# Kernel tuning notes

Hardware: AMD Instinct MI355X
Metric: run time of the kernel (lower is better)

Reference implementation:

```python
import jax, jax.numpy as jnp
import numpy as np

N = 8192
IN_DIM = 64
OUT_DIM = 64
HEADS = 2
EPS = 1e-10


def setup_inputs() -> dict:
    key = jax.random.key(0)
    ks = jax.random.split(key, 6)
    features = jax.random.normal(ks[0], (N, IN_DIM), dtype=jnp.float32)
    adj = (jax.random.uniform(ks[1], (N, N)) < 0.005).astype(jnp.float32)
    # per-head attention linear: Linear(2*in_dim, 1) stacked -> [heads, 2*in_dim]
    W_attn = jax.random.normal(ks[2], (HEADS, 2 * IN_DIM), dtype=jnp.float32) * 0.05
    b_attn = jax.random.normal(ks[3], (HEADS,), dtype=jnp.float32) * 0.05
    # feature transform: Linear(in_dim, heads*out_dim)
    W_lin = jax.random.normal(ks[4], (HEADS * OUT_DIM, IN_DIM), dtype=jnp.float32) * 0.05
    b_lin = jax.random.normal(ks[5], (HEADS * OUT_DIM,), dtype=jnp.float32) * 0.05
    return {"adj": adj, "features": features, "W_attn": W_attn,
            "b_attn": b_attn, "W_lin": W_lin, "b_lin": b_lin}


def reference(adj, features, W_attn, b_attn, W_lin, b_lin):
    n, in_dim = features.shape
    heads = W_attn.shape[0]
    # add self-loops (adj + sparse identity in the original)
    idx = jnp.arange(n)
    adj_sl = adj.at[idx, idx].add(1.0)
    # concat-based score: head([x_i ; x_j]) = x_i @ Wa_src + x_j @ Wa_dst + b
    # (avoids the O(N^2 * 2*in_dim) concat tensor the original materializes)
    s_src = features @ W_attn[:, :in_dim].T   # [N, H]
    s_dst = features @ W_attn[:, in_dim:].T   # [N, H]
    # scores[n,h,m] = exp(s_src[n,h] + s_dst[m,h] + b[h])
    scores = jnp.exp(s_src[:, :, None] + s_dst.T[None, :, :] + b_attn[None, :, None])
    scores = scores * adj_sl[:, None, :]                      # adjacency mask
    attn = scores / (jnp.sum(scores, axis=-1, keepdims=True) + EPS)
    # dropout is identity in eval mode (deterministic reference)
    ft = (features @ W_lin.T + b_lin).reshape(n, heads, -1)   # [N, H, OUT]
    out = jnp.einsum('nhm,mhj->nhj', attn, ft)                # aggregate neighbors
    return jax.nn.elu(out.reshape(n, -1))
```

## Files before the change

### kernel.cpp

```cpp
#include <hip/hip_runtime.h>
#include <math.h>

#define NN 8192
#define IN_DIM 64
#define GAT_EPS 1e-10f
#define EBUF_CAP 256

typedef float fvec4 __attribute__((ext_vector_type(4)));

__global__ void ft_kernel(const float* __restrict__ features,
                          const float* __restrict__ W_lin,
                          const float* __restrict__ b_lin,
                          float2* __restrict__ ftI) {
    int gid = blockIdx.x * blockDim.x + threadIdx.x;
    int n = gid >> 6;
    int c = gid & 63;
    const float4* f4 = (const float4*)(features + (size_t)n * IN_DIM);
    const float4* w0 = (const float4*)(W_lin + (size_t)c * IN_DIM);
    const float4* w1 = (const float4*)(W_lin + (size_t)(64 + c) * IN_DIM);
    float a0 = 0.f, a1 = 0.f;
#pragma unroll
    for (int d = 0; d < IN_DIM / 4; ++d) {
        float4 f = f4[d];
        float4 u = w0[d];
        float4 v = w1[d];
        a0 += f.x * u.x + f.y * u.y + f.z * u.z + f.w * u.w;
        a1 += f.x * v.x + f.y * v.y + f.z * v.z + f.w * v.w;
    }
    ftI[gid] = make_float2(a0 + b_lin[c], a1 + b_lin[64 + c]);
}

__global__ void score_kernel(const float* __restrict__ features,
                             const float* __restrict__ W_attn,
                             float2* __restrict__ pdv) {
    int n = blockIdx.x * blockDim.x + threadIdx.x;
    const float4* f4   = (const float4*)(features + (size_t)n * IN_DIM);
    const float4* wa0d = (const float4*)(W_attn + IN_DIM);
    const float4* wa1d = (const float4*)(W_attn + 3 * IN_DIM);
    float s0 = 0.f, s1 = 0.f;
#pragma unroll
    for (int d = 0; d < IN_DIM / 4; ++d) {
        float4 f = f4[d];
        float4 b = wa0d[d];
        float4 e = wa1d[d];
        s0 += f.x * b.x + f.y * b.y + f.z * b.z + f.w * b.w;
        s1 += f.x * e.x + f.y * e.y + f.z * e.z + f.w * e.w;
    }
    pdv[n] = make_float2(__expf(s0), __expf(s1));
}

__global__ void __launch_bounds__(256) gat_agg_kernel(
        const float* __restrict__ adj,
        const float2* __restrict__ ftI,
        const float2* __restrict__ pdv,
        float* __restrict__ out) {
    __shared__ int edges[4][EBUF_CAP];
    __shared__ int ecnt[4];
    int widx = threadIdx.x >> 6;
    int lane = threadIdx.x & 63;
    int n = blockIdx.x * 4 + widx;
    int* ebuf = edges[widx];

    if (lane == 0) ecnt[widx] = 0;

    const fvec4* arow = (const fvec4*)(adj + (size_t)n * NN) + lane;

#pragma unroll 1
    for (int it = 0; it < NN / 1024; ++it) {
        const fvec4* p = arow + it * 256;
        fvec4 v0 = __builtin_nontemporal_load(p);
        fvec4 v1 = __builtin_nontemporal_load(p + 64);
        fvec4 v2 = __builtin_nontemporal_load(p + 128);
        fvec4 v3 = __builtin_nontemporal_load(p + 192);
        unsigned mb = 0;
        mb |= (v0.x != 0.f) ? 0x0001u : 0u;
        mb |= (v0.y != 0.f) ? 0x0002u : 0u;
        mb |= (v0.z != 0.f) ? 0x0004u : 0u;
        mb |= (v0.w != 0.f) ? 0x0008u : 0u;
        mb |= (v1.x != 0.f) ? 0x0010u : 0u;
        mb |= (v1.y != 0.f) ? 0x0020u : 0u;
        mb |= (v1.z != 0.f) ? 0x0040u : 0u;
        mb |= (v1.w != 0.f) ? 0x0080u : 0u;
        mb |= (v2.x != 0.f) ? 0x0100u : 0u;
        mb |= (v2.y != 0.f) ? 0x0200u : 0u;
        mb |= (v2.z != 0.f) ? 0x0400u : 0u;
        mb |= (v2.w != 0.f) ? 0x0800u : 0u;
        mb |= (v3.x != 0.f) ? 0x1000u : 0u;
        mb |= (v3.y != 0.f) ? 0x2000u : 0u;
        mb |= (v3.z != 0.f) ? 0x4000u : 0u;
        mb |= (v3.w != 0.f) ? 0x8000u : 0u;
        if (mb) {
            int c = __popc(mb);
            int pos = atomicAdd(&ecnt[widx], c);
            int megabase = it * 1024 + lane * 4;
            while (mb) {
                int b = __ffs(mb) - 1;
                mb &= mb - 1;
                ebuf[pos++] = megabase + ((b >> 2) << 8) + (b & 3);
            }
        }
    }

    float2 ps = pdv[n];
    float2 fs = ftI[(size_t)n * 64 + lane];
    float acc0 = ps.x * fs.x, acc1 = ps.y * fs.y;
    float den0 = ps.x, den1 = ps.y;

    __syncthreads();

    int count = ecnt[widx];
    int e = 0;
    for (; e + 8 <= count; e += 8) {
        int4 ma = *(const int4*)&ebuf[e];
        int4 mbq = *(const int4*)&ebuf[e + 4];
        float2 p0 = pdv[ma.x],  p1 = pdv[ma.y],  p2 = pdv[ma.z],  p3 = pdv[ma.w];
        float2 p4 = pdv[mbq.x], p5 = pdv[mbq.y], p6 = pdv[mbq.z], p7 = pdv[mbq.w];
        float2 f0 = ftI[(size_t)ma.x * 64 + lane];
        float2 f1 = ftI[(size_t)ma.y * 64 + lane];
        float2 f2 = ftI[(size_t)ma.z * 64 + lane];
        float2 f3 = ftI[(size_t)ma.w * 64 + lane];
        float2 f4 = ftI[(size_t)mbq.x * 64 + lane];
        float2 f5 = ftI[(size_t)mbq.y * 64 + lane];
        float2 f6 = ftI[(size_t)mbq.z * 64 + lane];
        float2 f7 = ftI[(size_t)mbq.w * 64 + lane];
        acc0 += p0.x * f0.x + p1.x * f1.x + p2.x * f2.x + p3.x * f3.x
              + p4.x * f4.x + p5.x * f5.x + p6.x * f6.x + p7.x * f7.x;
        acc1 += p0.y * f0.y + p1.y * f1.y + p2.y * f2.y + p3.y * f3.y
              + p4.y * f4.y + p5.y * f5.y + p6.y * f6.y + p7.y * f7.y;
        den0 += p0.x + p1.x + p2.x + p3.x + p4.x + p5.x + p6.x + p7.x;
        den1 += p0.y + p1.y + p2.y + p3.y + p4.y + p5.y + p6.y + p7.y;
    }
    for (; e < count; ++e) {
        int m = ebuf[e];
        float2 p = pdv[m];
        float2 f = ftI[(size_t)m * 64 + lane];
        acc0 += p.x * f.x;
        acc1 += p.y * f.y;
        den0 += p.x;
        den1 += p.y;
    }

    float o0 = acc0 / (den0 + GAT_EPS);
    float o1 = acc1 / (den1 + GAT_EPS);
    o0 = o0 > 0.f ? o0 : expm1f(o0);
    o1 = o1 > 0.f ? o1 : expm1f(o1);
    out[(size_t)n * 128 + lane]      = o0;
    out[(size_t)n * 128 + 64 + lane] = o1;
}

extern "C" void kernel_launch(void* const* d_in, const int* in_sizes, int n_in,
                              void* d_out, int out_size, void* d_ws, size_t ws_size,
                              hipStream_t stream) {
    const float* adj      = (const float*)d_in[0];
    const float* features = (const float*)d_in[1];
    const float* W_attn   = (const float*)d_in[2];
    const float* W_lin    = (const float*)d_in[4];
    const float* b_lin    = (const float*)d_in[5];
    float* out = (float*)d_out;

    float* ws = (float*)d_ws;
    float2* ftI = (float2*)ws;
    float2* pdv = (float2*)(ws + (size_t)NN * 128);

    ft_kernel<<<(NN * 64) / 256, 256, 0, stream>>>(features, W_lin, b_lin, ftI);
    score_kernel<<<NN / 256, 256, 0, stream>>>(features, W_attn, pdv);
    gat_agg_kernel<<<NN / 4, 256, 0, stream>>>(adj, ftI, pdv, out);
}
```

Baseline: 404.7 us.

## Split adjacency scan into a separate fully parallel kernel writing global edge lists

The fused scan-plus-aggregate kernel, where each wave looped over a whole 8192-wide adjacency row, is split in two. A scan kernel gives each wave one 1024-column chunk and appends nonzero column indices to a per-row global edge list through global atomics. A separate aggregation kernel then loads each list into shared memory. This exposes far more memory-level parallelism for the 256 MB adjacency read, which dominates the runtime. The cost is two extra launches (one to zero the counters), a round trip of the edge lists through global memory, global atomics, and edge order that is no longer deterministic.

```diff
diff --git a/kernel.cpp b/kernel.cpp
--- a/kernel.cpp
+++ b/kernel.cpp
@@ -4,9 +4,13 @@
 #define NN 8192
 #define IN_DIM 64
 #define GAT_EPS 1e-10f
-#define EBUF_CAP 256
+#define ECAP 256
 
 typedef float fvec4 __attribute__((ext_vector_type(4)));
+
+__global__ void zero_cnt_kernel(int* __restrict__ cnt) {
+    cnt[blockIdx.x * blockDim.x + threadIdx.x] = 0;
+}
 
 __global__ void ft_kernel(const float* __restrict__ features,
                           const float* __restrict__ W_lin,
@@ -49,57 +53,63 @@
     pdv[n] = make_float2(__expf(s0), __expf(s1));
 }
 
-__global__ void __launch_bounds__(256) gat_agg_kernel(
-        const float* __restrict__ adj,
-        const float2* __restrict__ ftI,
-        const float2* __restrict__ pdv,
-        float* __restrict__ out) {
-    __shared__ int edges[4][EBUF_CAP];
-    __shared__ int ecnt[4];
+__global__ void __launch_bounds__(256) scan_kernel(const float* __restrict__ adj,
+                                                   int* __restrict__ cnt,
+                                                   int* __restrict__ elist) {
+    int wid  = (blockIdx.x * blockDim.x + threadIdx.x) >> 6;
+    int lane = threadIdx.x & 63;
+    int row   = wid >> 3;
+    int chunk = wid & 7;
+    const fvec4* p = (const fvec4*)(adj + (size_t)row * NN + chunk * 1024) + lane;
+    fvec4 v0 = __builtin_nontemporal_load(p);
+    fvec4 v1 = __builtin_nontemporal_load(p + 64);
+    fvec4 v2 = __builtin_nontemporal_load(p + 128);
+    fvec4 v3 = __builtin_nontemporal_load(p + 192);
+    unsigned mb = 0;
+    mb |= (v0.x != 0.f) ? 0x0001u : 0u;
+    mb |= (v0.y != 0.f) ? 0x0002u : 0u;
+    mb |= (v0.z != 0.f) ? 0x0004u : 0u;
+    mb |= (v0.w != 0.f) ? 0x0008u : 0u;
+    mb |= (v1.x != 0.f) ? 0x0010u : 0u;
+    mb |= (v1.y != 0.f) ? 0x0020u : 0u;
+    mb |= (v1.z != 0.f) ? 0x0040u : 0u;
+    mb |= (v1.w != 0.f) ? 0x0080u : 0u;
+    mb |= (v2.x != 0.f) ? 0x0100u : 0u;
+    mb |= (v2.y != 0.f) ? 0x0200u : 0u;
+    mb |= (v2.z != 0.f) ? 0x0400u : 0u;
+    mb |= (v2.w != 0.f) ? 0x0800u : 0u;
+    mb |= (v3.x != 0.f) ? 0x1000u : 0u;
+    mb |= (v3.y != 0.f) ? 0x2000u : 0u;
+    mb |= (v3.z != 0.f) ? 0x4000u : 0u;
+    mb |= (v3.w != 0.f) ? 0x8000u : 0u;
+    if (mb) {
+        int c = __popc(mb);
+        int pos = atomicAdd(&cnt[row], c);
+        int base = chunk * 1024 + lane * 4;
+        int* dst = elist + (size_t)row * ECAP;
+        while (mb) {
+            int b = __ffs(mb) - 1;
+            mb &= mb - 1;
+            if (pos < ECAP) dst[pos] = base + ((b >> 2) << 8) + (b & 3);
+            ++pos;
+        }
+    }
+}
+
+__global__ void __launch_bounds__(256) agg_kernel(const int* __restrict__ cnt,
+                                                  const int* __restrict__ elist,
+                                                  const float2* __restrict__ ftI,
+                                                  const float2* __restrict__ pdv,
+                                                  float* __restrict__ out) {
+    __shared__ int ebuf[4][ECAP];
     int widx = threadIdx.x >> 6;
     int lane = threadIdx.x & 63;
     int n = blockIdx.x * 4 + widx;
-    int* ebuf = edges[widx];
 
-    if (lane == 0) ecnt[widx] = 0;
-
-    const fvec4* arow = (const fvec4*)(adj + (size_t)n * NN) + lane;
-
-#pragma unroll 1
-    for (int it = 0; it < NN / 1024; ++it) {
-        const fvec4* p = arow + it * 256;
-        fvec4 v0 = __builtin_nontemporal_load(p);
-        fvec4 v1 = __builtin_nontemporal_load(p + 64);
-        fvec4 v2 = __builtin_nontemporal_load(p + 128);
-        fvec4 v3 = __builtin_nontemporal_load(p + 192);
-        unsigned mb = 0;
-        mb |= (v0.x != 0.f) ? 0x0001u : 0u;
-        mb |= (v0.y != 0.f) ? 0x0002u : 0u;
-        mb |= (v0.z != 0.f) ? 0x0004u : 0u;
-        mb |= (v0.w != 0.f) ? 0x0008u : 0u;
-        mb |= (v1.x != 0.f) ? 0x0010u : 0u;
-        mb |= (v1.y != 0.f) ? 0x0020u : 0u;
-        mb |= (v1.z != 0.f) ? 0x0040u : 0u;
-        mb |= (v1.w != 0.f) ? 0x0080u : 0u;
-        mb |= (v2.x != 0.f) ? 0x0100u : 0u;
-        mb |= (v2.y != 0.f) ? 0x0200u : 0u;
-        mb |= (v2.z != 0.f) ? 0x0400u : 0u;
-        mb |= (v2.w != 0.f) ? 0x0800u : 0u;
-        mb |= (v3.x != 0.f) ? 0x1000u : 0u;
-        mb |= (v3.y != 0.f) ? 0x2000u : 0u;
-        mb |= (v3.z != 0.f) ? 0x4000u : 0u;
-        mb |= (v3.w != 0.f) ? 0x8000u : 0u;
-        if (mb) {
-            int c = __popc(mb);
-            int pos = atomicAdd(&ecnt[widx], c);
-            int megabase = it * 1024 + lane * 4;
-            while (mb) {
-                int b = __ffs(mb) - 1;
-                mb &= mb - 1;
-                ebuf[pos++] = megabase + ((b >> 2) << 8) + (b & 3);
-            }
-        }
-    }
+    int count = cnt[n];
+    if (count > ECAP) count = ECAP;
+    const int* src = elist + (size_t)n * ECAP;
+    for (int e = lane; e < count; e += 64) ebuf[widx][e] = src[e];
 
     float2 ps = pdv[n];
     float2 fs = ftI[(size_t)n * 64 + lane];
@@ -108,11 +118,11 @@
 
     __syncthreads();
 
-    int count = ecnt[widx];
+    const int* eb = ebuf[widx];
     int e = 0;
     for (; e + 8 <= count; e += 8) {
-        int4 ma = *(const int4*)&ebuf[e];
-        int4 mbq = *(const int4*)&ebuf[e + 4];
+        int4 ma  = *(const int4*)&eb[e];
+        int4 mbq = *(const int4*)&eb[e + 4];
         float2 p0 = pdv[ma.x],  p1 = pdv[ma.y],  p2 = pdv[ma.z],  p3 = pdv[ma.w];
         float2 p4 = pdv[mbq.x], p5 = pdv[mbq.y], p6 = pdv[mbq.z], p7 = pdv[mbq.w];
         float2 f0 = ftI[(size_t)ma.x * 64 + lane];
@@ -131,7 +141,7 @@
         den1 += p0.y + p1.y + p2.y + p3.y + p4.y + p5.y + p6.y + p7.y;
     }
     for (; e < count; ++e) {
-        int m = ebuf[e];
+        int m = eb[e];
         float2 p = pdv[m];
         float2 f = ftI[(size_t)m * 64 + lane];
         acc0 += p.x * f.x;
@@ -159,10 +169,14 @@
     float* out = (float*)d_out;
 
     float* ws = (float*)d_ws;
-    float2* ftI = (float2*)ws;
-    float2* pdv = (float2*)(ws + (size_t)NN * 128);
+    float2* ftI  = (float2*)ws;
+    float2* pdv  = (float2*)(ws + (size_t)NN * 128);
+    int*    cnt  = (int*)(ws + (size_t)NN * 128 + 2 * NN);
+    int*    elst = cnt + NN;
 
+    zero_cnt_kernel<<<NN / 256, 256, 0, stream>>>(cnt);
     ft_kernel<<<(NN * 64) / 256, 256, 0, stream>>>(features, W_lin, b_lin, ftI);
     score_kernel<<<NN / 256, 256, 0, stream>>>(features, W_attn, pdv);
-    gat_agg_kernel<<<NN / 4, 256, 0, stream>>>(adj, ftI, pdv, out);
+    scan_kernel<<<(NN * 8) / 4, 256, 0, stream>>>(adj, cnt, elst);
+    agg_kernel<<<NN / 4, 256, 0, stream>>>(cnt, elst, ftI, pdv, out);
 }
```

Measured after the change: 480.8 us. 18.8% more time.
